# Kernel tuning notes

Hardware: AMD Instinct MI355X
Metric: run time of the kernel (lower is better)

## Reference

```python
import jax, jax.numpy as jnp
import numpy as np

B, S, D_IN, D_OUT = 8, 2048, 768, 768
SCALE = float(D_IN) ** 0.5  # module divides by embed_size**0.5 where embed_size = input_dim


def setup_inputs() -> dict:
    key = jax.random.key(0)
    ks = jax.random.split(key, 8)
    std = 1.0 / np.sqrt(D_IN)
    return {
        "x": jax.random.normal(ks[0], (B, S, D_IN), dtype=jnp.float32),
        "mask": jax.random.randint(ks[1], (B, S), 0, 2, dtype=jnp.int32),
        "Wq": jax.random.normal(ks[2], (D_OUT, D_IN), dtype=jnp.float32) * std,
        "bq": jax.random.normal(ks[3], (D_OUT,), dtype=jnp.float32) * std,
        "Wk": jax.random.normal(ks[4], (D_OUT, D_IN), dtype=jnp.float32) * std,
        "bk": jax.random.normal(ks[5], (D_OUT,), dtype=jnp.float32) * std,
        "Wv": jax.random.normal(ks[6], (D_OUT, D_IN), dtype=jnp.float32) * std,
        "bv": jax.random.normal(ks[7], (D_OUT,), dtype=jnp.float32) * std,
    }


def reference(x, mask, Wq, bq, Wk, bk, Wv, bv):
    # QKV projections: nn.Linear computes x @ W.T + b
    Q = jnp.einsum("bsd,od->bso", x, Wq) + bq  # [B,S,D_OUT]
    K = jnp.einsum("bsd,od->bso", x, Wk) + bk
    V = jnp.einsum("bsd,od->bso", x, Wv) + bv
    scores = jnp.einsum("bqo,bko->bqk", Q, K) / SCALE  # [B,S,S]
    # key-position mask broadcast over query dim
    scores = jnp.where(mask[:, None, :] == 0, -jnp.inf, scores)
    weights = jax.nn.softmax(scores, axis=-1)
    out = jnp.einsum("bqk,bko->bqo", weights, V)  # [B,S,D_OUT]
    return out.mean(axis=1, keepdims=True)  # [B,1,D_OUT]
```

## Files before the change

### kernel.cpp

```cpp
#include <hip/hip_runtime.h>
#include <hip/hip_bf16.h>


#define S 2048
#define DIM 768
#define BATCH 8

typedef __hip_bfloat16 bf16;
typedef __attribute__((ext_vector_type(8))) short bf16x8;
typedef __attribute__((ext_vector_type(4))) short short4v;
typedef __attribute__((ext_vector_type(4))) float f32x4;

__device__ __forceinline__ f32x4 mfma16(bf16x8 a, bf16x8 b, f32x4 c) {
  return __builtin_amdgcn_mfma_f32_16x16x32_bf16(a, b, c, 0, 0, 0);
}

__device__ __forceinline__ void load_lds16(const short* g, short* l) {
  __builtin_amdgcn_global_load_lds(
      (const __attribute__((address_space(1))) unsigned int*)g,
      (__attribute__((address_space(3))) unsigned int*)l, 16, 0, 0);
}

__device__ __forceinline__ float b2f(short u) {
  union { float f; unsigned u; } v;
  v.u = ((unsigned)(unsigned short)u) << 16;
  return v.f;
}

__device__ __forceinline__ short f2b(float f) {
  bf16 h = __float2bfloat16(f);
  return *(short*)&h;
}

#define INV_SCALE 0.03608439182435161f

__global__ __launch_bounds__(256) void detect_dtype(const unsigned short* __restrict__ x,
                                                    int* __restrict__ flag) {
  int bad = 0;
  for (int i = threadIdx.x; i < 2048; i += 256) {
    int e = (x[i] >> 7) & 0xFF;
    if (e < 0x60 || e >= 0x9F) bad = 1;
  }
  if (bad) atomicOr(flag, 1);
}

__global__ __launch_bounds__(256) void prep_kernel(const void* __restrict__ Wq_raw,
                                                   const void* __restrict__ Wk_raw,
                                                   const void* __restrict__ bq_raw,
                                                   bf16* __restrict__ T0,
                                                   bf16* __restrict__ T1,
                                                   float* __restrict__ bvec,
                                                   const int* __restrict__ flag) {
  const int f = *flag;
  const int bx = blockIdx.x;
  if (bx < 288) {
    __shared__ unsigned short tile[64][66];
    const int p = bx / 144, r = bx % 144;
    const void* src = p ? Wk_raw : Wq_raw;
    unsigned short* dst = (unsigned short*)(p ? T1 : T0);
    const int obase = (r / 12) * 64, ibase = (r % 12) * 64;
    const int col = threadIdx.x & 63, rq = threadIdx.x >> 6;
#pragma unroll
    for (int rr = 0; rr < 64; rr += 4) {
      const long idx = (long)(obase + rr + rq) * DIM + ibase + col;
      const float v = f ? ((const float*)src)[idx] : b2f(((const short*)src)[idx]);
      tile[rr + rq][col] = (unsigned short)f2b(v);
    }
    __syncthreads();
#pragma unroll
    for (int rr = 0; rr < 64; rr += 4)
      dst[(long)(ibase + rr + rq) * DIM + obase + col] = tile[col][rr + rq];
  } else {
    const int o0 = (bx - 288) * 128;
    const int t = threadIdx.x;
    float s0 = 0.f, s1 = 0.f, s2 = 0.f;
    if (f) {
      const float* W = (const float*)Wk_raw;
      const float* bq = (const float*)bq_raw;
      for (int o = o0; o < o0 + 128; ++o) {
        const float bo = bq[o];
        const float* row = W + (long)o * DIM;
        s0 += row[t] * bo;
        s1 += row[t + 256] * bo;
        s2 += row[t + 512] * bo;
      }
    } else {
      const short* W = (const short*)Wk_raw;
      const short* bq = (const short*)bq_raw;
      for (int o = o0; o < o0 + 128; ++o) {
        const float bo = b2f(bq[o]);
        const short* row = W + (long)o * DIM;
        s0 += b2f(row[t]) * bo;
        s1 += b2f(row[t + 256]) * bo;
        s2 += b2f(row[t + 512]) * bo;
      }
    }
    atomicAdd(&bvec[t], s0);
    atomicAdd(&bvec[t + 256], s1);
    atomicAdd(&bvec[t + 512], s2);
  }
}

#define TILE_DECLS                                                          \
  __shared__ short As[4096], Bs[4096];                                      \
  const int tid = threadIdx.x;                                              \
  const int wave = tid >> 6, lane = tid & 63;                               \
  const int lr = lane & 15, quad = lane >> 4;                               \
  const int wm = (wave >> 1) * 64, wn = (wave & 1) * 64;                    \
  const int c0row = tid >> 2, colw = (tid & 3) * 8;

#define TILE_KLOOP(Abase, Bbase)                                            \
  const short* Ag0 = (Abase) + (long)(mblk + c0row) * DIM + colw;           \
  const short* Ag1 = (Abase) + (long)(mblk + 64 + c0row) * DIM + colw;      \
  const short* Bg0 = (Bbase) + (long)(nblk + c0row) * DIM + colw;           \
  const short* Bg1 = (Bbase) + (long)(nblk + 64 + c0row) * DIM + colw;      \
  short* Al0 = As + tid * 8;                                                \
  short* Al1 = As + 2048 + tid * 8;                                         \
  short* Bl0 = Bs + tid * 8;                                                \
  short* Bl1 = Bs + 2048 + tid * 8;                                         \
  f32x4 acc[4][4] = {};                                                     \
  for (int k0 = 0; k0 < DIM; k0 += 32) {                                    \
    load_lds16(Ag0 + k0, Al0);                                              \
    load_lds16(Ag1 + k0, Al1);                                              \
    load_lds16(Bg0 + k0, Bl0);                                              \
    load_lds16(Bg1 + k0, Bl1);                                              \
    asm volatile("s_waitcnt vmcnt(0)" ::: "memory");                        \
    __syncthreads();                                                        \
    bf16x8 af[4], bfr[4];                                                   \
    _Pragma("unroll") for (int it = 0; it < 4; ++it)                        \
        af[it] = *(const bf16x8*)(As + (wm + it * 16 + lr) * 32 + quad * 8);\
    _Pragma("unroll") for (int jt = 0; jt < 4; ++jt)                        \
        bfr[jt] = *(const bf16x8*)(Bs + (wn + jt * 16 + lr) * 32 + quad * 8);\
    _Pragma("unroll") for (int it = 0; it < 4; ++it)                        \
        _Pragma("unroll") for (int jt = 0; jt < 4; ++jt)                    \
            acc[it][jt] = mfma16(af[it], bfr[jt], acc[it][jt]);             \
    __syncthreads();                                                        \
  }

__global__ __launch_bounds__(256) void mt_convert(const bf16* __restrict__ WkT,
                                                  const bf16* __restrict__ WqT,
                                                  bf16* __restrict__ Mt,
                                                  const void* __restrict__ x_raw,
                                                  const int* __restrict__ mask,
                                                  const float* __restrict__ bvec,
                                                  bf16* __restrict__ xb,
                                                  float* __restrict__ betas,
                                                  const int* __restrict__ flag) {
  const int bx = blockIdx.x;
  if (bx < 36) {
    const int mblk = (bx / 6) * 128, nblk = (bx % 6) * 128;
    TILE_DECLS
    TILE_KLOOP((const short*)WkT, (const short*)WqT)
#pragma unroll
    for (int it = 0; it < 4; ++it)
#pragma unroll
      for (int jt = 0; jt < 4; ++jt)
#pragma unroll
        for (int r = 0; r < 4; ++r)
          Mt[(long)(mblk + wm + it * 16 + quad * 4 + r) * DIM +
             nblk + wn + jt * 16 + lr] = __float2bfloat16(acc[it][jt][r]);
  } else {
    const int wave = threadIdx.x >> 6, lane = threadIdx.x & 63;
    const int n = (bx - 36) * 4 + wave;
    const int f = *flag;
    short* xo = (short*)xb + (long)n * DIM;
    float s = 0.f;
    if (f) {
      const float4* x4 = (const float4*)((const float*)x_raw + (long)n * DIM);
      const float4* bv4 = (const float4*)bvec;
#pragma unroll
      for (int it = 0; it < 3; ++it) {
        const int idx = it * 64 + lane;
        const float4 v = x4[idx];
        const float4 bb = bv4[idx];
        short4v sv = {f2b(v.x), f2b(v.y), f2b(v.z), f2b(v.w)};
        *(short4v*)(xo + idx * 4) = sv;
        s += v.x * bb.x + v.y * bb.y + v.z * bb.z + v.w * bb.w;
      }
    } else {
      const short4v* x4 = (const short4v*)((const short*)x_raw + (long)n * DIM);
      const float4* bv4 = (const float4*)bvec;
#pragma unroll
      for (int it = 0; it < 3; ++it) {
        const int idx = it * 64 + lane;
        const short4v v = x4[idx];
        const float4 bb = bv4[idx];
        *(short4v*)(xo + idx * 4) = v;
        s += b2f(v.x) * bb.x + b2f(v.y) * bb.y + b2f(v.z) * bb.z + b2f(v.w) * bb.w;
      }
    }
#pragma unroll
    for (int off = 1; off < 64; off <<= 1) s += __shfl_xor(s, off, 64);
    if (lane == 0) betas[n] = mask[n] ? s * INV_SCALE : -1e30f;
  }
}


#define BARX() asm volatile("s_barrier" ::: "memory")
#define LGKM0() asm volatile("s_waitcnt lgkmcnt(0)" ::: "memory")
#define VMC4() asm volatile("s_waitcnt vmcnt(4)" ::: "memory")
#define VMC0() asm volatile("s_waitcnt vmcnt(0)" ::: "memory")

__device__ __forceinline__ void core256(const short* A, const short* B,
                                        short* sh, f32x4 (&acc)[8][4],
                                        const int wm, const int wn,
                                        const int lr, const int quad,
                                        const int tid) {
  const int sw7 = lr & 7;
  const int cof0 = (quad ^ sw7) * 8;
  const int cof1 = ((quad + 4) ^ sw7) * 8;
  const int rS = tid >> 3;
  const int cS8 = ((tid & 7) ^ (rS & 7)) * 8;
  const short* aP0 = A + (long)rS * DIM + cS8;
  const short* aP1 = aP0 + 128 * DIM;
  const short* bP0 = B + (long)rS * DIM + cS8;
  const short* bP1 = bP0 + 128 * DIM;
  short* l0 = sh + tid * 8;
  short* l1 = sh + 4096 + tid * 8;
  bf16x8 af0[4][2], af1[4][2], bf0[2][2], bf1[2][2];

#define STG(BASE, GP, K0)                              \
  do {                                                 \
    load_lds16((GP) + (K0), l0 + (BASE));              \
    load_lds16((GP) + 64 * DIM + (K0), l1 + (BASE));   \
  } while (0)
#define READ_AF0(AB)                                                \
  _Pragma("unroll") for (int f_ = 0; f_ < 4; ++f_) {                \
    const int ro_ = (AB) + (wm + f_ * 16 + lr) * 64;                \
    af0[f_][0] = *(const bf16x8*)(sh + ro_ + cof0);                 \
    af0[f_][1] = *(const bf16x8*)(sh + ro_ + cof1);                 \
  }
#define READ_AF1(AB)                                                \
  _Pragma("unroll") for (int f_ = 0; f_ < 4; ++f_) {                \
    const int ro_ = (AB) + (wm + 64 + f_ * 16 + lr) * 64;           \
    af1[f_][0] = *(const bf16x8*)(sh + ro_ + cof0);                 \
    af1[f_][1] = *(const bf16x8*)(sh + ro_ + cof1);                 \
  }
#define READ_BF0(BB)                                                \
  _Pragma("unroll") for (int f_ = 0; f_ < 2; ++f_) {                \
    const int ro_ = (BB) + (wn + f_ * 16 + lr) * 64;                \
    bf0[f_][0] = *(const bf16x8*)(sh + ro_ + cof0);                 \
    bf0[f_][1] = *(const bf16x8*)(sh + ro_ + cof1);                 \
  }
#define READ_BF1(BB)                                                \
  _Pragma("unroll") for (int f_ = 0; f_ < 2; ++f_) {                \
    const int ro_ = (BB) + (wn + 32 + f_ * 16 + lr) * 64;           \
    bf1[f_][0] = *(const bf16x8*)(sh + ro_ + cof0);                 \
    bf1[f_][1] = *(const bf16x8*)(sh + ro_ + cof1);                 \
  }
#define MMA8(AF, BF, FIO, FJO)                                            \
  _Pragma("unroll") for (int i_ = 0; i_ < 4; ++i_)                        \
  _Pragma("unroll") for (int j_ = 0; j_ < 2; ++j_) {                      \
    acc[i_ + (FIO)][j_ + (FJO)] =                                         \
        mfma16(AF[i_][0], BF[j_][0], acc[i_ + (FIO)][j_ + (FJO)]);        \
    acc[i_ + (FIO)][j_ + (FJO)] =                                         \
        mfma16(AF[i_][1], BF[j_][1], acc[i_ + (FIO)][j_ + (FJO)]);        \
  }

  STG(16384, bP0, 0); STG(24576, bP1, 0);
  STG(0, aP0, 0);     STG(8192, aP1, 0);
  STG(49152, bP0, 64); STG(57344, bP1, 64);
  VMC4();
  BARX();

#pragma unroll 1
  for (int t = 0; t < 5; ++t) {
    const int kA1 = (2 * t + 1) * 64;
    const int kB2 = kA1 + 64;
    const int kB3 = kB2 + 64;
    READ_AF0(0) READ_BF0(16384)
    STG(32768, aP0, kA1);
    BARX(); LGKM0(); __builtin_amdgcn_s_setprio(1);
    MMA8(af0, bf0, 0, 0) __builtin_amdgcn_s_setprio(0); BARX();
    READ_BF1(16384)
    STG(40960, aP1, kA1);
    BARX(); LGKM0(); __builtin_amdgcn_s_setprio(1);
    MMA8(af0, bf1, 0, 2) __builtin_amdgcn_s_setprio(0); BARX();
    READ_AF1(0)
    STG(16384, bP0, kB2);
    BARX(); LGKM0(); __builtin_amdgcn_s_setprio(1);
    MMA8(af1, bf0, 4, 0) __builtin_amdgcn_s_setprio(0); BARX();
    STG(24576, bP1, kB2);
    VMC4();
    BARX(); __builtin_amdgcn_s_setprio(1);
    MMA8(af1, bf1, 4, 2) __builtin_amdgcn_s_setprio(0); BARX();
    READ_AF0(32768) READ_BF0(49152)
    STG(0, aP0, kB2);
    BARX(); LGKM0(); __builtin_amdgcn_s_setprio(1);
    MMA8(af0, bf0, 0, 0) __builtin_amdgcn_s_setprio(0); BARX();
    READ_BF1(49152)
    STG(8192, aP1, kB2);
    BARX(); LGKM0(); __builtin_amdgcn_s_setprio(1);
    MMA8(af0, bf1, 0, 2) __builtin_amdgcn_s_setprio(0); BARX();
    READ_AF1(32768)
    STG(49152, bP0, kB3);
    BARX(); LGKM0(); __builtin_amdgcn_s_setprio(1);
    MMA8(af1, bf0, 4, 0) __builtin_amdgcn_s_setprio(0); BARX();
    STG(57344, bP1, kB3);
    VMC4();
    BARX(); __builtin_amdgcn_s_setprio(1);
    MMA8(af1, bf1, 4, 2) __builtin_amdgcn_s_setprio(0); BARX();
  }

  READ_AF0(0) READ_BF0(16384)
  STG(32768, aP0, 704);
  BARX(); LGKM0(); __builtin_amdgcn_s_setprio(1);
  MMA8(af0, bf0, 0, 0) __builtin_amdgcn_s_setprio(0); BARX();
  READ_BF1(16384)
  STG(40960, aP1, 704);
  BARX(); LGKM0(); __builtin_amdgcn_s_setprio(1);
  MMA8(af0, bf1, 0, 2) __builtin_amdgcn_s_setprio(0); BARX();
  READ_AF1(0)
  BARX(); LGKM0(); __builtin_amdgcn_s_setprio(1);
  MMA8(af1, bf0, 4, 0) __builtin_amdgcn_s_setprio(0); BARX();
  VMC0();
  BARX(); __builtin_amdgcn_s_setprio(1);
  MMA8(af1, bf1, 4, 2) __builtin_amdgcn_s_setprio(0); BARX();
  READ_AF0(32768) READ_BF0(49152)
  BARX(); LGKM0(); __builtin_amdgcn_s_setprio(1);
  MMA8(af0, bf0, 0, 0) __builtin_amdgcn_s_setprio(0); BARX();
  READ_BF1(49152)
  BARX(); LGKM0(); __builtin_amdgcn_s_setprio(1);
  MMA8(af0, bf1, 0, 2) __builtin_amdgcn_s_setprio(0); BARX();
  READ_AF1(32768)
  BARX(); LGKM0(); __builtin_amdgcn_s_setprio(1);
  MMA8(af1, bf0, 4, 0) __builtin_amdgcn_s_setprio(0); BARX();
  __builtin_amdgcn_s_setprio(1);
  MMA8(af1, bf1, 4, 2) __builtin_amdgcn_s_setprio(0);

#undef STG
#undef READ_AF0
#undef READ_AF1
#undef READ_BF0
#undef READ_BF1
#undef MMA8
}

__global__ __launch_bounds__(512, 2) void gemm_nt_256(const bf16* __restrict__ A,
                                                      const bf16* __restrict__ B,
                                                      bf16* __restrict__ D) {
  __shared__ __align__(16) short sh[65536];
  const int tid = threadIdx.x;
  const int wave = tid >> 6, lane = tid & 63;
  const int lr = lane & 15, quad = lane >> 4;
  const int wm = (wave >> 2) * 128, wn = (wave & 3) * 64;
  const int mblk = blockIdx.x * 256, nblk = blockIdx.y * 256;
  f32x4 acc[8][4] = {};
  core256((const short*)A + (long)mblk * DIM, (const short*)B + (long)nblk * DIM,
          sh, acc, wm, wn, lr, quad, tid);
#pragma unroll
  for (int fi = 0; fi < 8; ++fi)
#pragma unroll
    for (int fj = 0; fj < 4; ++fj)
#pragma unroll
      for (int r = 0; r < 4; ++r)
        D[(long)(mblk + wm + fi * 16 + quad * 4 + r) * DIM +
          nblk + wn + fj * 16 + lr] = __float2bfloat16(acc[fi][fj][r]);
}

__global__ __launch_bounds__(512, 2) void gemm_pass1(const bf16* __restrict__ z,
                                                     const bf16* __restrict__ x,
                                                     const float* __restrict__ betas,
                                                     float* __restrict__ l_out,
                                                     int b0) {
  __shared__ __align__(16) short sh[65536];
  const int nwg = (int)gridDim.x;
  const int cpx = nwg >> 3;
  const int bid = (blockIdx.x & 7) * cpx + (blockIdx.x >> 3);
  const int lb = bid >> 6, rb = bid & 63;
  const int mblk = (rb >> 3) * 256, nblk = (rb & 7) * 256;
  const int b = b0 + lb;
  const int tid = threadIdx.x;
  const int wave = tid >> 6, lane = tid & 63;
  const int lr = lane & 15, quad = lane >> 4;
  const int wm = (wave >> 2) * 128, wn = (wave & 3) * 64;
  f32x4 acc[8][4] = {};
  core256((const short*)z + (long)lb * S * DIM + (long)mblk * DIM,
          (const short*)x + (long)b * S * DIM + (long)nblk * DIM,
          sh, acc, wm, wn, lr, quad, tid);
  float bet[4];
#pragma unroll
  for (int fj = 0; fj < 4; ++fj)
    bet[fj] = betas[b * S + nblk + wn + fj * 16 + lr];
  float* lrow = l_out + b * S;
#pragma unroll
  for (int fi = 0; fi < 8; ++fi) {
#pragma unroll
    for (int r = 0; r < 4; ++r) {
      const int q = mblk + wm + fi * 16 + quad * 4 + r;
      float s = 0.f;
#pragma unroll
      for (int fj = 0; fj < 4; ++fj)
        s += __expf(fminf(acc[fi][fj][r] * INV_SCALE + bet[fj], 60.f));
      s += __shfl_xor(s, 1, 64);
      s += __shfl_xor(s, 2, 64);
      s += __shfl_xor(s, 4, 64);
      s += __shfl_xor(s, 8, 64);
      if (lr == 0) atomicAdd(&lrow[q], s);
    }
  }
}

__global__ __launch_bounds__(512, 2) void gemm_pass2(const bf16* __restrict__ z,
                                                     const bf16* __restrict__ x,
                                                     const float* __restrict__ betas,
                                                     const float* __restrict__ l,
                                                     float* __restrict__ c,
                                                     int b0) {
  __shared__ __align__(16) short sh[65536];
  const int nwg = (int)gridDim.x;
  const int cpx = nwg >> 3;
  const int bid = (blockIdx.x & 7) * cpx + (blockIdx.x >> 3);
  const int lb = bid >> 6, rb = bid & 63;
  const int mblk = (rb >> 3) * 256, nblk = (rb & 7) * 256;
  const int b = b0 + lb;
  const int tid = threadIdx.x;
  const int wave = tid >> 6, lane = tid & 63;
  const int lr = lane & 15, quad = lane >> 4;
  const int wm = (wave >> 2) * 128, wn = (wave & 3) * 64;
  f32x4 acc[8][4] = {};
  core256((const short*)z + (long)lb * S * DIM + (long)mblk * DIM,
          (const short*)x + (long)b * S * DIM + (long)nblk * DIM,
          sh, acc, wm, wn, lr, quad, tid);
  float* lds_rq = (float*)sh;
  float* cred = (float*)sh + 256;
  if (tid < 256) {
    const float lv = l[b * S + mblk + tid];
    lds_rq[tid] = lv > 0.f ? 1.0f / lv : 0.f;
  }
  float bet[4];
#pragma unroll
  for (int fj = 0; fj < 4; ++fj)
    bet[fj] = betas[b * S + nblk + wn + fj * 16 + lr];
  __syncthreads();
  float csum[4] = {};
#pragma unroll
  for (int fi = 0; fi < 8; ++fi) {
#pragma unroll
    for (int r = 0; r < 4; ++r) {
      const float rqv = lds_rq[wm + fi * 16 + quad * 4 + r];
#pragma unroll
      for (int fj = 0; fj < 4; ++fj)
        csum[fj] += __expf(fminf(acc[fi][fj][r] * INV_SCALE + bet[fj], 60.f)) * rqv;
    }
  }
#pragma unroll
  for (int fj = 0; fj < 4; ++fj) {
    csum[fj] += __shfl_xor(csum[fj], 16, 64);
    csum[fj] += __shfl_xor(csum[fj], 32, 64);
  }
  if (wave >= 4 && quad == 0) {
#pragma unroll
    for (int fj = 0; fj < 4; ++fj)
      cred[((wave & 3) * 4 + fj) * 16 + lr] = csum[fj];
  }
  __syncthreads();
  if (wave < 4 && quad == 0) {
#pragma unroll
    for (int fj = 0; fj < 4; ++fj)
      atomicAdd(&c[b * S + nblk + wn + fj * 16 + lr],
                (csum[fj] + cred[(wave * 4 + fj) * 16 + lr]) * (1.0f / 2048.0f));
  }
}

__global__ __launch_bounds__(256) void y_kernel(const bf16* __restrict__ x,
                                                const float* __restrict__ c,
                                                float* __restrict__ y) {
  const int b = blockIdx.z;
  const int i = blockIdx.x * 256 + threadIdx.x;
  const int kstart = blockIdx.y * 128;
  const bf16* xb = x + (long)(b * S + kstart) * DIM + i;
  const float* cb = c + b * S + kstart;
  float acc = 0.f;
  for (int k = 0; k < 128; ++k)
    acc += cb[k] * __bfloat162float(xb[(long)k * DIM]);
  atomicAdd(&y[b * DIM + i], acc);
}

__global__ __launch_bounds__(256) void out_kernel(const float* __restrict__ y,
                                                  const void* __restrict__ Wv_raw,
                                                  const void* __restrict__ bv_raw,
                                                  void* __restrict__ out,
                                                  const int* __restrict__ flag) {
  const int wave = threadIdx.x >> 6, lane = threadIdx.x & 63;
  const int w = blockIdx.x * 4 + wave;
  const int b = w / DIM, o = w % DIM;
  const int f = *flag;
  const float4* y4 = (const float4*)(y + (long)b * DIM);
  float s = 0.f;
  if (f) {
    const float4* wr = (const float4*)((const float*)Wv_raw + (long)o * DIM);
#pragma unroll
    for (int it = 0; it < 3; ++it) {
      const int idx = it * 64 + lane;
      const float4 a = y4[idx], wv = wr[idx];
      s += a.x * wv.x + a.y * wv.y + a.z * wv.z + a.w * wv.w;
    }
  } else {
    const short4v* wr = (const short4v*)((const short*)Wv_raw + (long)o * DIM);
#pragma unroll
    for (int it = 0; it < 3; ++it) {
      const int idx = it * 64 + lane;
      const float4 a = y4[idx];
      const short4v wv = wr[idx];
      s += a.x * b2f(wv.x) + a.y * b2f(wv.y) + a.z * b2f(wv.z) + a.w * b2f(wv.w);
    }
  }
#pragma unroll
  for (int off = 1; off < 64; off <<= 1) s += __shfl_xor(s, off, 64);
  if (lane == 0) {
    const float bias = f ? ((const float*)bv_raw)[o] : b2f(((const short*)bv_raw)[o]);
    const float v = s + bias;
    if (f) ((float*)out)[b * DIM + o] = v;
    else ((bf16*)out)[b * DIM + o] = __float2bfloat16(v);
  }
}

extern "C" void kernel_launch(void* const* d_in, const int* in_sizes, int n_in,
                              void* d_out, int out_size, void* d_ws, size_t ws_size,
                              hipStream_t stream) {
  const void* x_raw = d_in[0];
  const int* mask = (const int*)d_in[1];
  const void* Wq_raw = d_in[2];
  const void* bq_raw = d_in[3];
  const void* Wk_raw = d_in[4];
  const void* Wv_raw = d_in[6];
  const void* bv_raw = d_in[7];

  char* ws = (char*)d_ws;
  bf16* xb = (bf16*)(ws);
  bf16* WqT = (bf16*)(ws + 25165824);
  bf16* WkT = (bf16*)(ws + 26345472);
  bf16* Mt = (bf16*)(ws + 27525120);
  float* betas = (float*)(ws + 28704768);
  float* bvec = (float*)(ws + 28770304);
  float* l = (float*)(ws + 28773376);
  float* c = (float*)(ws + 28838912);
  float* y = (float*)(ws + 28904448);
  int* flag = (int*)(ws + 28929024);
  bf16* z = (bf16*)(ws + 28929088);

  const size_t fixed = 28929088;
  const size_t zb = 3145728;
  int nb = 1;
  if (ws_size >= fixed + 8 * zb) nb = 8;
  else if (ws_size >= fixed + 4 * zb) nb = 4;
  else if (ws_size >= fixed + 2 * zb) nb = 2;
  const int rounds = BATCH / nb;

  (void)hipMemsetAsync(bvec, 0, 3072 + 65536 + 65536 + 24576 + 64, stream);

  detect_dtype<<<1, 256, 0, stream>>>((const unsigned short*)x_raw, flag);
  prep_kernel<<<294, 256, 0, stream>>>(Wq_raw, Wk_raw, bq_raw, WqT, WkT, bvec, flag);
  mt_convert<<<4132, 256, 0, stream>>>(WkT, WqT, Mt, x_raw, mask, bvec, xb,
                                       betas, flag);

  for (int r = 0; r < rounds; ++r) {
    const int b0 = r * nb;
    gemm_nt_256<<<dim3(nb * 8, 3), 512, 0, stream>>>(
        xb + (long)b0 * S * DIM, Mt, z);
    gemm_pass1<<<nb * 64, 512, 0, stream>>>(z, xb, betas, l, b0);
    gemm_pass2<<<nb * 64, 512, 0, stream>>>(z, xb, betas, l, c, b0);
  }

  y_kernel<<<dim3(3, 16, 8), 256, 0, stream>>>(xb, c, y);
  out_kernel<<<1536, 256, 0, stream>>>(y, Wv_raw, bv_raw, d_out, flag);
}
```

Before: 270.1 us.

## Fuse score GEMM passes with inter-block row-sum barrier to avoid recomputing scores

Merges the two score-GEMM passes into one kernel. Each workgroup computes its score tile once, atomically adds its row sums, then spin-waits on a per-row-block counter until all 8 column tiles have contributed, and reuses the register accumulators for the normalized column sums. This removes the second full GEMM recomputation. In exchange it relies on all co-dependent workgroups being resident at once, which is why batches per round drop from 8 to 4, and it adds spin-wait and atomic-read overhead.

```diff
diff --git a/kernel.cpp b/kernel.cpp
--- a/kernel.cpp
+++ b/kernel.cpp
@@ -358,11 +358,13 @@
           nblk + wn + fj * 16 + lr] = __float2bfloat16(acc[fi][fj][r]);
 }
 
-__global__ __launch_bounds__(512, 2) void gemm_pass1(const bf16* __restrict__ z,
-                                                     const bf16* __restrict__ x,
-                                                     const float* __restrict__ betas,
-                                                     float* __restrict__ l_out,
-                                                     int b0) {
+__global__ __launch_bounds__(512, 2) void gemm_score_fused(const bf16* __restrict__ z,
+                                                           const bf16* __restrict__ x,
+                                                           const float* __restrict__ betas,
+                                                           float* __restrict__ l_out,
+                                                           float* __restrict__ c,
+                                                           int* __restrict__ cnt,
+                                                           int b0) {
   __shared__ __align__(16) short sh[65536];
   const int nwg = (int)gridDim.x;
   const int cpx = nwg >> 3;
@@ -399,39 +401,23 @@
       if (lr == 0) atomicAdd(&lrow[q], s);
     }
   }
-}
-
-__global__ __launch_bounds__(512, 2) void gemm_pass2(const bf16* __restrict__ z,
-                                                     const bf16* __restrict__ x,
-                                                     const float* __restrict__ betas,
-                                                     const float* __restrict__ l,
-                                                     float* __restrict__ c,
-                                                     int b0) {
-  __shared__ __align__(16) short sh[65536];
-  const int nwg = (int)gridDim.x;
-  const int cpx = nwg >> 3;
-  const int bid = (blockIdx.x & 7) * cpx + (blockIdx.x >> 3);
-  const int lb = bid >> 6, rb = bid & 63;
-  const int mblk = (rb >> 3) * 256, nblk = (rb & 7) * 256;
-  const int b = b0 + lb;
-  const int tid = threadIdx.x;
-  const int wave = tid >> 6, lane = tid & 63;
-  const int lr = lane & 15, quad = lane >> 4;
-  const int wm = (wave >> 2) * 128, wn = (wave & 3) * 64;
-  f32x4 acc[8][4] = {};
-  core256((const short*)z + (long)lb * S * DIM + (long)mblk * DIM,
-          (const short*)x + (long)b * S * DIM + (long)nblk * DIM,
-          sh, acc, wm, wn, lr, quad, tid);
+  asm volatile("s_waitcnt vmcnt(0)" ::: "memory");
+  __threadfence();
+  __syncthreads();
+  int* cp = cnt + b * 8 + (rb >> 3);
+  if (tid == 0) {
+    const int prev = atomicAdd(cp, 1);
+    if (prev + 1 < 8) {
+      while (atomicAdd(cp, 0) < 8) __builtin_amdgcn_s_sleep(8);
+    }
+  }
+  __syncthreads();
   float* lds_rq = (float*)sh;
   float* cred = (float*)sh + 256;
   if (tid < 256) {
-    const float lv = l[b * S + mblk + tid];
+    const float lv = atomicAdd(&l_out[b * S + mblk + tid], 0.0f);
     lds_rq[tid] = lv > 0.f ? 1.0f / lv : 0.f;
   }
-  float bet[4];
-#pragma unroll
-  for (int fj = 0; fj < 4; ++fj)
-    bet[fj] = betas[b * S + nblk + wn + fj * 16 + lr];
   __syncthreads();
   float csum[4] = {};
 #pragma unroll
@@ -538,17 +524,17 @@
   float* c = (float*)(ws + 28838912);
   float* y = (float*)(ws + 28904448);
   int* flag = (int*)(ws + 28929024);
-  bf16* z = (bf16*)(ws + 28929088);
-
-  const size_t fixed = 28929088;
+  int* cnt = (int*)(ws + 28929088);
+  bf16* z = (bf16*)(ws + 28929344);
+
+  const size_t fixed = 28929344;
   const size_t zb = 3145728;
   int nb = 1;
-  if (ws_size >= fixed + 8 * zb) nb = 8;
-  else if (ws_size >= fixed + 4 * zb) nb = 4;
+  if (ws_size >= fixed + 4 * zb) nb = 4;
   else if (ws_size >= fixed + 2 * zb) nb = 2;
   const int rounds = BATCH / nb;
 
-  (void)hipMemsetAsync(bvec, 0, 3072 + 65536 + 65536 + 24576 + 64, stream);
+  (void)hipMemsetAsync(bvec, 0, 3072 + 65536 + 65536 + 24576 + 64 + 256, stream);
 
   detect_dtype<<<1, 256, 0, stream>>>((const unsigned short*)x_raw, flag);
   prep_kernel<<<294, 256, 0, stream>>>(Wq_raw, Wk_raw, bq_raw, WqT, WkT, bvec, flag);
@@ -559,8 +545,7 @@
     const int b0 = r * nb;
     gemm_nt_256<<<dim3(nb * 8, 3), 512, 0, stream>>>(
         xb + (long)b0 * S * DIM, Mt, z);
-    gemm_pass1<<<nb * 64, 512, 0, stream>>>(z, xb, betas, l, b0);
-    gemm_pass2<<<nb * 64, 512, 0, stream>>>(z, xb, betas, l, c, b0);
+    gemm_score_fused<<<nb * 64, 512, 0, stream>>>(z, xb, betas, l, c, cnt, b0);
   }
 
   y_kernel<<<dim3(3, 16, 8), 256, 0, stream>>>(xb, c, y);
```

After: 314.8 us. 16.5% more time.
